# Performance work log

Measured on AMD Instinct MI355X. Metric: run time of the kernel, lower is better.

Reference implementation:

```python
import jax, jax.numpy as jnp
import numpy as np

B = 4096          # sum(hierchy_struc) time series
L = 32            # number of hierarchy levels = len(hierchy_struc)
D = 512           # d_model
DQK = 512         # d_model_qk
DV = 512          # d_model_v
H = 8             # heads
HIER = [128] * 32 # hierchy_struc
GROUP = np.repeat(np.arange(L), HIER)  # group id of each batch row, shape [B]


def setup_inputs() -> dict:
    key = jax.random.key(0)
    ks = jax.random.split(key, 9)
    s_in = 1.0 / np.sqrt(D)
    s_v = 1.0 / np.sqrt(DV)
    return {
        "x": jax.random.normal(ks[0], (B, L, D), jnp.float32),
        "Wq": jax.random.normal(ks[1], (D, DQK), jnp.float32) * s_in,
        "bq": jax.random.normal(ks[2], (DQK,), jnp.float32) * s_in,
        "Wk": jax.random.normal(ks[3], (D, DQK), jnp.float32) * s_in,
        "bk": jax.random.normal(ks[4], (DQK,), jnp.float32) * s_in,
        "Wv": jax.random.normal(ks[5], (D, DV), jnp.float32) * s_in,
        "bv": jax.random.normal(ks[6], (DV,), jnp.float32) * s_in,
        "Wo": jax.random.normal(ks[7], (DV, DV), jnp.float32) * s_v,
        "bo": jax.random.normal(ks[8], (DV,), jnp.float32) * s_v,
    }


def reference(x, Wq, bq, Wk, bk, Wv, bv, Wo, bo):
    # QKV projections -> (B, H, L, dh)
    def split_heads(y):
        b, l, d = y.shape
        return y.reshape(b, l, H, d // H).transpose(0, 2, 1, 3)

    q = split_heads(x @ Wq + bq)
    k = split_heads(x @ Wk + bk)
    v = split_heads(x @ Wv + bv)

    dh = q.shape[-1]
    scores = jnp.einsum("bhqd,bhkd->bhqk", q, k) / float(np.sqrt(dh))
    p_attn = jax.nn.softmax(scores, axis=-1)  # (B, H, L, L)

    # hierarchical post-softmax mask: batch row b only keeps query row GROUP[b]
    group = jnp.asarray(GROUP)
    row_keep = (jnp.arange(L)[None, :] == group[:, None]).astype(p_attn.dtype)
    p_attn = p_attn * row_keep[:, None, :, None]

    ctx = jnp.einsum("bhqk,bhkd->bhqd", p_attn, v)          # (B, H, L, dh)
    ctx = ctx.transpose(0, 2, 1, 3).reshape(B, L, DV)        # merge heads

    # p_attn.sum(dim=2) -> (B,H,L); transpose(1,2) -> (B,L,H); mean(dim=2) -> (B,L)
    p_attn_sum = p_attn.sum(axis=2).mean(axis=1)

    out = ctx @ Wo + bo
    return out, p_attn_sum
```

## Files before the change

kernel.cpp:

```cpp
#include <hip/hip_runtime.h>
#include <hip/hip_bf16.h>
#include <math.h>

typedef unsigned short u16;
typedef __attribute__((ext_vector_type(2))) float f32x2;
typedef __attribute__((ext_vector_type(4))) float f32x4;
typedef __attribute__((ext_vector_type(4))) unsigned short u16x4;
typedef __attribute__((ext_vector_type(8))) short s16x8;
typedef __attribute__((ext_vector_type(2))) unsigned int u32x2;
typedef __attribute__((ext_vector_type(4))) unsigned int u32x4;

__device__ __forceinline__ u16 f2bf(float f) {
  union { float f; unsigned int u; } v; v.f = f;
  unsigned int r = v.u + 0x7FFFu + ((v.u >> 16) & 1u);
  return (u16)(r >> 16);
}
__device__ __forceinline__ float bf2f(u16 u) {
  union { unsigned int u; float f; } v; v.u = ((unsigned int)u) << 16;
  return v.f;
}
__device__ __forceinline__ float u2f(unsigned int u) {
  union { unsigned int u; float f; } v; v.u = u;
  return v.f;
}
__device__ __forceinline__ void gload16(const void* g, void* l) {
  __builtin_amdgcn_global_load_lds(
      (const __attribute__((address_space(1))) unsigned int*)g,
      (__attribute__((address_space(3))) unsigned int*)l, 16, 0, 0);
}

__global__ __launch_bounds__(256)
void fill_kernel(const float* __restrict__ bo, float* __restrict__ out)
{
  const int gid = blockIdx.x * 256 + threadIdx.x;
  const f32x4 bov = ((const f32x4*)bo)[gid & 127];
  f32x4* o4 = (f32x4*)out;
#pragma unroll
  for (int it = 0; it < 32; ++it)
    __builtin_nontemporal_store(bov, &o4[gid + it * 524288]);
}

__global__ __launch_bounds__(256)
void prep_kernel(const float* __restrict__ x,
                 const float* __restrict__ Wq, const float* __restrict__ Wv,
                 const float* __restrict__ Wo, const float* __restrict__ Wk,
                 u16* __restrict__ wqT, u16* __restrict__ wvT,
                 u16* __restrict__ woT, u16* __restrict__ wkB,
                 u16* __restrict__ xg)
{
  const int blk = blockIdx.x;
  const int t = threadIdx.x;
  if (blk < 192) {
    __shared__ u16 tile[64 * 72];
    int m = blk >> 6, tno = blk & 63;
    const float* W = (m == 0) ? Wq : (m == 1) ? Wv : Wo;
    u16* WT = (m == 0) ? wqT : (m == 1) ? wvT : woT;
    int r0 = (tno >> 3) * 64, c0 = (tno & 7) * 64;
    int tr = t >> 4;
    int tc = (t & 15) * 4;
#pragma unroll
    for (int ii = 0; ii < 4; ii++) {
      int r = tr + ii * 16;
      f32x4 v = *(const f32x4*)(W + (long)(r0 + r) * 512 + c0 + tc);
#pragma unroll
      for (int j = 0; j < 4; j++) tile[(tc + j) * 72 + r] = f2bf(v[j]);
    }
    __syncthreads();
#pragma unroll
    for (int ii = 0; ii < 4; ii++) {
      int r = tr + ii * 16;
      u16x4 o;
#pragma unroll
      for (int j = 0; j < 4; j++) o[j] = tile[r * 72 + tc + j];
      *(u16x4*)(WT + (long)(c0 + r) * 512 + r0 + tc) = o;
    }
  } else if (blk < 448) {
    int i = (blk - 192) * 256 + t;
    f32x4 v = *(const f32x4*)(Wk + (long)i * 4);
    u16x4 o;
#pragma unroll
    for (int j = 0; j < 4; j++) o[j] = f2bf(v[j]);
    *(u16x4*)(wkB + (long)i * 4) = o;
  } else {
    int i = (blk - 448) * 256 + t;
    int bb = i >> 7, d = (i & 127) * 4;
    int g = bb >> 7;
    f32x4 v = *(const f32x4*)(x + ((long)bb * 32 + g) * 512 + d);
    u16x4 o;
#pragma unroll
    for (int j = 0; j < 4; j++) o[j] = f2bf(v[j]);
    *(u16x4*)(xg + (long)bb * 512 + d) = o;
  }
}

template<int BM, int BN, bool OUT_BF16, bool CROW_REMAP, bool ADD_BIAS>
__global__ __launch_bounds__(256)
void gemm_tn(const u16* __restrict__ A, int lda, long aZ,
             const u16* __restrict__ B, int ldb, long bZ,
             void* __restrict__ Cv, int ldc, long cZ,
             const float* __restrict__ bias, int biasZ, int K)
{
  constexpr int BK = 64;
  constexpr int CS = BN + 8;
  constexpr int STG = BM * BK + BN * BK;
  constexpr int SMEM = (STG > BM * CS) ? STG : BM * CS;
  __shared__ u16 smem[SMEM];
  u16* As = smem;
  u16* Bs = smem + BM * BK;
  const int z = blockIdx.z;
  const u16* Ab = A + (long)z * aZ + (long)blockIdx.y * BM * lda;
  const u16* Bb = B + (long)z * bZ + (long)blockIdx.x * BN * ldb;
  const int tid = threadIdx.x;
  const int wave = tid >> 6, lane = tid & 63;
  constexpr int WM = BM / 2, WN = BN / 2;
  const int wm = wave >> 1, wn = wave & 1;
  constexpr int MF = WM / 16, NF = WN / 16;
  constexpr int ACH = (BM * BK * 2) / 1024;
  constexpr int BCH = (BN * BK * 2) / 1024;
  f32x4 acc[MF][NF] = {};
  const int rIn  = lane >> 3;
  const int cOff = (lane & 7) * 8;

  for (int kb = 0; kb < K; kb += BK) {
#pragma unroll
    for (int ch = 0; ch < ACH / 4; ch++) {
      int c = wave + ch * 4;
      int r = c * 8 + rIn;
      gload16(Ab + (long)r * lda + kb + cOff, As + c * 512 + lane * 8);
    }
#pragma unroll
    for (int ch = 0; ch < BCH / 4; ch++) {
      int c = wave + ch * 4;
      int r = c * 8 + rIn;
      gload16(Bb + (long)r * ldb + kb + cOff, Bs + c * 512 + lane * 8);
    }
    __syncthreads();
#pragma unroll
    for (int ks = 0; ks < BK; ks += 32) {
      s16x8 af[MF], bfv[NF];
#pragma unroll
      for (int i = 0; i < MF; i++)
        af[i] = *(const s16x8*)(As + (wm * WM + i * 16 + (lane & 15)) * BK + ks + ((lane >> 4) * 8));
#pragma unroll
      for (int j = 0; j < NF; j++)
        bfv[j] = *(const s16x8*)(Bs + (wn * WN + j * 16 + (lane & 15)) * BK + ks + ((lane >> 4) * 8));
#pragma unroll
      for (int i = 0; i < MF; i++)
#pragma unroll
        for (int j = 0; j < NF; j++)
          acc[i][j] = __builtin_amdgcn_mfma_f32_16x16x32_bf16(af[i], bfv[j], acc[i][j], 0, 0, 0);
    }
    __syncthreads();
  }

  const long cz = (long)z * cZ;
  if constexpr (OUT_BF16) {
#pragma unroll
    for (int j = 0; j < NF; j++) {
      int colL = wn * WN + j * 16 + (lane & 15);
      float bvv = 0.f;
      if (ADD_BIAS) bvv = bias[(long)z * biasZ + blockIdx.x * BN + colL];
#pragma unroll
      for (int i = 0; i < MF; i++) {
#pragma unroll
        for (int r4 = 0; r4 < 4; r4++) {
          int rowL = wm * WM + i * 16 + ((lane >> 4) << 2) + r4;
          smem[rowL * CS + colL] = f2bf(acc[i][j][r4] + bvv);
        }
      }
    }
    __syncthreads();
    constexpr int CPR = BN / 8;
    constexpr int CHUNKS = BM * CPR;
    u16* Cb = (u16*)Cv + cz + (long)blockIdx.y * BM * ldc + blockIdx.x * BN;
#pragma unroll 4
    for (int c = tid; c < CHUNKS; c += 256) {
      int row = c / CPR, co = (c % CPR) * 8;
      s16x8 vv = *(const s16x8*)(smem + row * CS + co);
      *(s16x8*)(Cb + (long)row * ldc + co) = vv;
    }
  } else {
    const int colBase = blockIdx.x * BN + wn * WN;
    const int rowBase = blockIdx.y * BM + wm * WM;
#pragma unroll
    for (int j = 0; j < NF; j++) {
      int col = colBase + j * 16 + (lane & 15);
      float bvv = 0.f;
      if (ADD_BIAS) bvv = bias[(long)z * biasZ + col];
#pragma unroll
      for (int i = 0; i < MF; i++) {
#pragma unroll
        for (int r4 = 0; r4 < 4; r4++) {
          int row = rowBase + i * 16 + ((lane >> 4) << 2) + r4;
          float v = acc[i][j][r4] + bvv;
          if constexpr (CROW_REMAP) {
            ((float*)Cv)[((long)row * 32 + (row >> 7)) * ldc + col] = v;
          } else {
            ((float*)Cv)[cz + (long)row * ldc + col] = v;
          }
        }
      }
    }
  }
}

#define PSUM_OFF 67108864L

__global__ __launch_bounds__(256)
void attn_kernel(const float* __restrict__ x, u16* __restrict__ QKY,
                 float* __restrict__ out)
{
  const int b = blockIdx.x;
  const int t = threadIdx.x;
  const int wave = t >> 6, lane = t & 63;
  __shared__ u16 xs[16384];
  __shared__ float scl[32 * 8];
  __shared__ float pl[8 * 32];

  const f32x4* x4 = (const f32x4*)(x + (long)b * 16384);
#pragma unroll
  for (int it = 0; it < 16; ++it) {
    int i = t + it * 256;
    int l = (i & 3) * 8 + (i >> 9);
    int dq = (i >> 2) & 127;
    f32x4 v = __builtin_nontemporal_load(&x4[l * 128 + dq]);
    u16x4 uv;
    uv[0] = f2bf(v[0]); uv[1] = f2bf(v[1]); uv[2] = f2bf(v[2]); uv[3] = f2bf(v[3]);
    int S = ((l >> 2) << 5) + (dq >> 2);
    int off = (S << 6) + ((l & 3) << 4) + ((((dq & 3) << 2)) ^ ((S & 1) << 3));
    *(u16x4*)(xs + off) = uv;
  }
  __syncthreads();

  if (wave < 2) {
    const int l0 = wave * 16;
    const int arow = l0 + (lane & 15);
    const int brow = lane & 15;
    const u16* qkg = QKY + (long)b * 4096;
    f32x4 acc = {0.f, 0.f, 0.f, 0.f};
#pragma unroll
    for (int ks = 0; ks < 16; ks++) {
      int d0 = ks * 32 + (lane >> 4) * 8;
      int S = ((arow >> 2) << 5) + (d0 >> 4);
      int aoff = (S << 6) + ((arow & 3) << 4) + ((d0 & 15) ^ ((S & 1) << 3));
      s16x8 af = *(const s16x8*)(xs + aoff);
      s16x8 bf = *(const s16x8*)(qkg + brow * 512 + d0);
      acc = __builtin_amdgcn_mfma_f32_16x16x32_bf16(af, bf, acc, 0, 0, 0);
    }
    if (brow < 8) {
#pragma unroll
      for (int r = 0; r < 4; r++)
        scl[(l0 + (lane >> 4) * 4 + r) * 8 + brow] = acc[r] * 0.125f;
    }
  }
  __syncthreads();

  const int h = t >> 5, l = t & 31;
  {
    float s = scl[l * 8 + h];
    float m = s;
#pragma unroll
    for (int mk = 16; mk; mk >>= 1) m = fmaxf(m, __shfl_xor(m, mk, 32));
    float ex = expf(s - m);
    float sum = ex;
#pragma unroll
    for (int mk = 16; mk; mk >>= 1) sum += __shfl_xor(sum, mk, 32);
    pl[h * 32 + l] = ex / sum;
  }
  __syncthreads();
  if (t < 32) {
    float ps = 0.f;
#pragma unroll
    for (int hh = 0; hh < 8; hh++) ps += pl[hh * 32 + t];
    out[PSUM_OFF + (long)b * 32 + t] = ps * 0.125f;
  }
  f32x2 a0p[4] = {}, a1p[4] = {};
  const int dbase = (t & 31) * 16;
  const int stag = (t >> 2) & 3;
#pragma unroll 4
  for (int i2 = 0; i2 < 32; i2++) {
    int ll = (i2 + stag) & 31;
    float pv = pl[h * 32 + ll];
    f32x2 pv2 = {pv, pv};
    int S0 = ((ll >> 2) << 5) + (t & 31);
    int base = (S0 << 6) + ((ll & 3) << 4);
    int sw = (S0 & 1) << 3;
    u32x4 xa = *(const u32x4*)(xs + base + sw);
    u32x4 xc = *(const u32x4*)(xs + base + (8 ^ sw));
#pragma unroll
    for (int e2 = 0; e2 < 4; e2++) {
      f32x2 xp0, xp1;
      xp0[0] = u2f(xa[e2] << 16); xp0[1] = u2f(xa[e2] & 0xFFFF0000u);
      xp1[0] = u2f(xc[e2] << 16); xp1[1] = u2f(xc[e2] & 0xFFFF0000u);
      a0p[e2] += xp0 * pv2;
      a1p[e2] += xp1 * pv2;
    }
  }
  u16* yrow = QKY + (long)b * 4096 + h * 512 + dbase;
  s16x8 o0, o1;
#pragma unroll
  for (int e2 = 0; e2 < 4; e2++) {
    o0[e2 * 2]     = (short)f2bf(a0p[e2][0]);
    o0[e2 * 2 + 1] = (short)f2bf(a0p[e2][1]);
    o1[e2 * 2]     = (short)f2bf(a1p[e2][0]);
    o1[e2 * 2 + 1] = (short)f2bf(a1p[e2][1]);
  }
  *(s16x8*)(yrow) = o0;
  *(s16x8*)(yrow + 8) = o1;
}

extern "C" void kernel_launch(void* const* d_in, const int* in_sizes, int n_in,
                              void* d_out, int out_size, void* d_ws, size_t ws_size,
                              hipStream_t stream)
{
  const float* x  = (const float*)d_in[0];
  const float* Wq = (const float*)d_in[1];
  const float* bq = (const float*)d_in[2];
  const float* Wk = (const float*)d_in[3];
  const float* Wv = (const float*)d_in[5];
  const float* bv = (const float*)d_in[6];
  const float* Wo = (const float*)d_in[7];
  const float* bo = (const float*)d_in[8];
  float* out = (float*)d_out;

  char* w = (char*)d_ws;
  u16* wqT = (u16*)(w);
  u16* wkB = (u16*)(w + 524288);
  u16* wvT = (u16*)(w + 1048576);
  u16* woT = (u16*)(w + 1572864);
  u16* xg  = (u16*)(w + 2097152);
  u16* qbf = (u16*)(w + 6291456);
  u16* qky = (u16*)(w + 10485760);
  u16* ctx = (u16*)(w + 44040192);

  fill_kernel<<<2048, 256, 0, stream>>>(bo, out);
  prep_kernel<<<2496, 256, 0, stream>>>(x, Wq, Wv, Wo, Wk, wqT, wvT, woT, wkB, xg);
  gemm_tn<64, 64, true, false, true><<<dim3(8, 64, 1), 256, 0, stream>>>(
      xg, 512, 0, wqT, 512, 0, qbf, 512, 0, bq, 0, 512);
  gemm_tn<128, 128, true, false, false><<<dim3(4, 32, 8), 256, 0, stream>>>(
      qbf, 512, 64, wkB, 512, 64, qky, 4096, 512, nullptr, 0, 64);
  attn_kernel<<<4096, 256, 0, stream>>>(x, qky, out);
  gemm_tn<64, 64, true, false, true><<<dim3(1, 64, 8), 256, 0, stream>>>(
      qky, 4096, 512, wvT, 512, 32768, ctx, 512, 64, bv, 64, 512);
  gemm_tn<64, 64, false, true, true><<<dim3(8, 64, 1), 256, 0, stream>>>(
      ctx, 512, 0, woT, 512, 0, out, 512, 0, bo, 0, 512);
}
```

Before: 181.1 us.

## Fuse bias fill into attention kernel and split score MFMA across all waves

Removes the separate fill_kernel that wrote bo into the full output and instead has each attention block write the bias rows for its own batch element. The score MFMA loop, previously run by two waves, is now split along the K dimension across all four waves, with partial sums combined in shared memory before the softmax. This saves a kernel launch and a full pass over the output, and shortens the serial score computation, at the cost of an extra shared buffer and more store traffic inside the attention kernel.

```diff
diff --git a/kernel.cpp b/kernel.cpp
--- a/kernel.cpp
+++ b/kernel.cpp
@@ -7,7 +7,6 @@
 typedef __attribute__((ext_vector_type(4))) float f32x4;
 typedef __attribute__((ext_vector_type(4))) unsigned short u16x4;
 typedef __attribute__((ext_vector_type(8))) short s16x8;
-typedef __attribute__((ext_vector_type(2))) unsigned int u32x2;
 typedef __attribute__((ext_vector_type(4))) unsigned int u32x4;
 
 __device__ __forceinline__ u16 f2bf(float f) {
@@ -27,17 +26,6 @@
   __builtin_amdgcn_global_load_lds(
       (const __attribute__((address_space(1))) unsigned int*)g,
       (__attribute__((address_space(3))) unsigned int*)l, 16, 0, 0);
-}
-
-__global__ __launch_bounds__(256)
-void fill_kernel(const float* __restrict__ bo, float* __restrict__ out)
-{
-  const int gid = blockIdx.x * 256 + threadIdx.x;
-  const f32x4 bov = ((const f32x4*)bo)[gid & 127];
-  f32x4* o4 = (f32x4*)out;
-#pragma unroll
-  for (int it = 0; it < 32; ++it)
-    __builtin_nontemporal_store(bov, &o4[gid + it * 524288]);
 }
 
 __global__ __launch_bounds__(256)
@@ -208,16 +196,25 @@
 
 __global__ __launch_bounds__(256)
 void attn_kernel(const float* __restrict__ x, u16* __restrict__ QKY,
-                 float* __restrict__ out)
+                 const float* __restrict__ bo, float* __restrict__ out)
 {
   const int b = blockIdx.x;
   const int t = threadIdx.x;
   const int wave = t >> 6, lane = t & 63;
   __shared__ u16 xs[16384];
-  __shared__ float scl[32 * 8];
+  __shared__ float sclp[2][32 * 8];
   __shared__ float pl[8 * 32];
 
   const f32x4* x4 = (const f32x4*)(x + (long)b * 16384);
+  {
+    const f32x4* bo4 = (const f32x4*)bo;
+    f32x4* ob = (f32x4*)(out + (long)b * 16384);
+#pragma unroll
+    for (int it = 0; it < 16; ++it) {
+      int i = t + it * 256;
+      __builtin_nontemporal_store(bo4[i & 127], &ob[i]);
+    }
+  }
 #pragma unroll
   for (int it = 0; it < 16; ++it) {
     int i = t + it * 256;
@@ -232,15 +229,16 @@
   }
   __syncthreads();
 
-  if (wave < 2) {
-    const int l0 = wave * 16;
+  {
+    const int kw = wave >> 1, lw = wave & 1;
+    const int l0 = lw * 16;
     const int arow = l0 + (lane & 15);
     const int brow = lane & 15;
     const u16* qkg = QKY + (long)b * 4096;
     f32x4 acc = {0.f, 0.f, 0.f, 0.f};
 #pragma unroll
-    for (int ks = 0; ks < 16; ks++) {
-      int d0 = ks * 32 + (lane >> 4) * 8;
+    for (int ksi = 0; ksi < 8; ksi++) {
+      int d0 = (kw * 8 + ksi) * 32 + (lane >> 4) * 8;
       int S = ((arow >> 2) << 5) + (d0 >> 4);
       int aoff = (S << 6) + ((arow & 3) << 4) + ((d0 & 15) ^ ((S & 1) << 3));
       s16x8 af = *(const s16x8*)(xs + aoff);
@@ -250,14 +248,14 @@
     if (brow < 8) {
 #pragma unroll
       for (int r = 0; r < 4; r++)
-        scl[(l0 + (lane >> 4) * 4 + r) * 8 + brow] = acc[r] * 0.125f;
+        sclp[kw][(l0 + (lane >> 4) * 4 + r) * 8 + brow] = acc[r];
     }
   }
   __syncthreads();
 
   const int h = t >> 5, l = t & 31;
   {
-    float s = scl[l * 8 + h];
+    float s = (sclp[0][l * 8 + h] + sclp[1][l * 8 + h]) * 0.125f;
     float m = s;
 #pragma unroll
     for (int mk = 16; mk; mk >>= 1) m = fmaxf(m, __shfl_xor(m, mk, 32));
@@ -333,13 +331,12 @@
   u16* qky = (u16*)(w + 10485760);
   u16* ctx = (u16*)(w + 44040192);
 
-  fill_kernel<<<2048, 256, 0, stream>>>(bo, out);
   prep_kernel<<<2496, 256, 0, stream>>>(x, Wq, Wv, Wo, Wk, wqT, wvT, woT, wkB, xg);
   gemm_tn<64, 64, true, false, true><<<dim3(8, 64, 1), 256, 0, stream>>>(
       xg, 512, 0, wqT, 512, 0, qbf, 512, 0, bq, 0, 512);
   gemm_tn<128, 128, true, false, false><<<dim3(4, 32, 8), 256, 0, stream>>>(
       qbf, 512, 64, wkB, 512, 64, qky, 4096, 512, nullptr, 0, 64);
-  attn_kernel<<<4096, 256, 0, stream>>>(x, qky, out);
+  attn_kernel<<<4096, 256, 0, stream>>>(x, qky, bo, out);
   gemm_tn<64, 64, true, false, true><<<dim3(1, 64, 8), 256, 0, stream>>>(
       qky, 4096, 512, wvT, 512, 32768, ctx, 512, 64, bv, 64, 512);
   gemm_tn<64, 64, false, true, true><<<dim3(8, 64, 1), 256, 0, stream>>>(
```

Measured after the change: 159.0 us. 12.2% less time.
